# Kernel optimization log

Hardware: AMD Instinct MI355X
Metric: run time of the kernel (lower is better)

## Reference

```python
import jax, jax.numpy as jnp
import numpy as np

LAM = 0.7      # lambda_param
GAM = 2.0      # gamma (weight upper bound)
ALPHA = 0.1    # age modulation scale
FGAM = 0.1     # fusion_gamma
SIGMAS = jnp.array([0.1, 0.5, 1.0, 2.0], dtype=jnp.float32)  # multi-kernel sigmas


def setup_inputs() -> dict:
    key = jax.random.key(0)
    ks = jax.random.split(key, 12)
    B, C, D, H, W, K = 12, 64, 32, 32, 32, 32
    mid, red = C // 2, C // 4
    Z = jax.random.normal(ks[0], (B, C, D, H, W), jnp.float32)
    masks = (jax.random.uniform(ks[1], (K, D, H, W)) > 0.5).astype(jnp.float32)
    masks = masks.at[:, 0, 0, 0].set(1.0)  # guarantee every region non-empty
    labels = jnp.arange(B, dtype=jnp.int32) % 3  # 4 samples each of CN/MCI/AD
    ages = 50.0 + 40.0 * jax.random.uniform(ks[2], (B,), jnp.float32)
    prior_weights = 1.0 + 0.1 * jax.random.normal(ks[3], (K,), jnp.float32)
    struct_w = 0.05 * jax.random.normal(ks[4], (mid, C), jnp.float32)
    noise_w = 0.05 * jax.random.normal(ks[5], (mid, C), jnp.float32)
    up_w = 0.05 * jax.random.normal(ks[6], (C, mid), jnp.float32)
    region_w = 0.05 * jax.random.normal(ks[7], (C, C, 3, 3, 3), jnp.float32)
    m_w1 = 0.05 * jax.random.normal(ks[8], (red, C), jnp.float32)
    m_b1 = jnp.zeros((red,), jnp.float32)
    m_w2 = 0.05 * jax.random.normal(ks[9], (C, red), jnp.float32)
    m_b2 = jnp.zeros((C,), jnp.float32)
    return dict(Z=Z, masks=masks, labels=labels, ages=ages, prior_weights=prior_weights,
                struct_w=struct_w, noise_w=noise_w, up_w=up_w, region_w=region_w,
                m_w1=m_w1, m_b1=m_b1, m_w2=m_w2, m_b2=m_b2)


def _mmd_pair(kern, ca, cb):
    # kern: [S,K,B,B] RBF kernels; ca/cb: [B] float class indicators.
    # Unbiased MMD^2 per region, averaged over sigmas -> [K].
    m = ca.sum()
    n = cb.sum()
    Kaa = jnp.einsum('skij,i,j->sk', kern, ca, ca)
    da = jnp.einsum('skii,i->sk', kern, ca)
    Kbb = jnp.einsum('skij,i,j->sk', kern, cb, cb)
    db = jnp.einsum('skii,i->sk', kern, cb)
    t1 = (Kaa - da) / (m * (m - 1.0))
    t2 = (Kbb - db) / (n * (n - 1.0))
    t3 = jnp.einsum('skij,i,j->sk', kern, ca, cb) * (-2.0 / (m * n))
    return (t1 + t2 + t3).mean(0)


def _forward(Z, masks, labels, ages, prior_weights, struct_w, noise_w, up_w,
             region_w, m_w1, m_b1, m_w2, m_b2):
    B, C = Z.shape[:2]
    K = masks.shape[0]
    # --- region-specific aggregation (fused segment-reduce over masks) ---
    msum = masks.sum((1, 2, 3))                                   # [K]
    rf = jnp.einsum('bcdhw,kdhw->bkc', Z, masks) / (msum[None, :, None] + 1e-6)
    # --- multi-class multi-kernel MMD per region ---
    x2 = jnp.sum(rf * rf, -1)                                     # [B,K]
    ip = jnp.einsum('ikc,jkc->kij', rf, rf)                       # [K,B,B]
    d2 = jnp.maximum(x2.T[:, :, None] + x2.T[:, None, :] - 2.0 * ip, 0.0)
    kern = jnp.exp(-d2[None] / (2.0 * SIGMAS[:, None, None, None] ** 2))  # [S,K,B,B]
    c_cn = (labels == 0).astype(jnp.float32)
    c_mci = (labels == 1).astype(jnp.float32)
    c_ad = (labels == 2).astype(jnp.float32)
    D_mmd = (_mmd_pair(kern, c_ad, c_cn) + _mmd_pair(kern, c_mci, c_cn)
             + _mmd_pair(kern, c_ad, c_mci))                      # [K]
    max_mmd = jnp.maximum(D_mmd.max(), 1e-6)
    nm = jnp.clip(D_mmd / max_mmd, 0.0)
    # symmetric KL between prior and MMD-evidence distributions (batchmean -> /K)
    lp = jax.nn.log_softmax(prior_weights)
    lq = jax.nn.log_softmax(nm)
    p = jnp.exp(lp)
    q = jnp.exp(lq)
    reg = 0.5 * jnp.sum(q * (lq - lp)) / K + 0.5 * jnp.sum(p * (lp - lq)) / K
    # --- prior-guided adaptive spatial weights ---
    base = LAM * prior_weights + (1.0 - LAM) * nm
    af = 1.0 + jax.nn.softplus(ALPHA * (ages - 50.0))             # [B]
    Wk = jax.nn.softmax(jnp.clip(base[None, :] * af[:, None], 0.0, GAM), axis=1)
    spatial = jnp.einsum('bk,kdhw->bdhw', Wk, masks)[:, None]     # [B,1,D,H,W]
    # --- orthogonal decomposition ---
    cs = jnp.einsum('oc,bcdhw->bodhw', struct_w, Z)               # 1x1x1 conv
    cnoise = jnp.einsum('oc,bcdhw->bodhw', noise_w, Z)
    s = cs.reshape(B, cs.shape[1], -1)
    n = cnoise.reshape(B, cnoise.shape[1], -1)
    eps = 1e-8
    cos = jnp.sum(s * n, -1) / (jnp.maximum(jnp.linalg.norm(s, axis=-1), eps)
                                * jnp.maximum(jnp.linalg.norm(n, axis=-1), eps))
    ortho = jnp.abs(cos).mean()
    Z_clean = jnp.einsum('oc,bcdhw->bodhw', up_w, cs)
    # --- region base field + 3x3x3 conv + channel modulation ---
    Zrb = jnp.einsum('bkc,kdhw->bcdhw', rf, masks)
    Zrec = jax.lax.conv_general_dilated(
        Zrb, region_w, (1, 1, 1), 'SAME',
        dimension_numbers=('NCDHW', 'OIDHW', 'NCDHW'))
    h = jax.nn.relu(jnp.einsum('bkc,rc->bkr', rf, m_w1) + m_b1)
    mod = jax.nn.softplus(jnp.einsum('bkr,cr->bkc', h, m_w2) + m_b2)  # [B,K,C]
    Zmod = Zrec * jnp.einsum('bkc,kdhw->bcdhw', mod, masks)
    Z_out = Z_clean + FGAM * (Zmod * spatial)
    return rf, spatial, Z_out, reg + ortho


def reference(Z, masks, labels, ages, prior_weights, struct_w, noise_w, up_w,
              region_w, m_w1, m_b1, m_w2, m_b2):
    return _forward(Z, masks, labels, ages, prior_weights, struct_w, noise_w,
                    up_w, region_w, m_w1, m_b1, m_w2, m_b2)
```

## Files before the change

### kernel.cpp

```cpp
#include <hip/hip_runtime.h>
#include <hip/hip_bf16.h>
#include <math.h>

#define REG_OFF    0
#define ORTHO_OFF  1
#define FLAG_OFF   2
#define MSUM_OFF   4
#define RF_OFF     64
#define G_OFF      24640
#define WKW_OFF    73792
#define MODTB_OFF  74176
#define M1TTH_OFF  86464
#define M1TTL_OFF  88512
#define WKCB_OFF   90560
#define IPK_OFF    422336
#define WS_TOTAL   426944
#define ZERO_FLOATS 73792

#define RF_OUT   0
#define SPAT_OUT 24576
#define ZOUT_OUT 417792
#define SCAL_OUT 25583616

typedef unsigned short u16;
typedef short bh8 __attribute__((ext_vector_type(8)));
typedef float fv4 __attribute__((ext_vector_type(4)));

__device__ __forceinline__ float bf2f(u16 u) {
  union { unsigned int i; float f; } x; x.i = ((unsigned int)u) << 16; return x.f;
}
__device__ __forceinline__ u16 f2bf(float f) {
  unsigned int u = __float_as_uint(f);
  return (u16)((u + 0x7fffu + ((u >> 16) & 1u)) >> 16);
}
__device__ __forceinline__ float ldin(const void* p, size_t i, bool f32) {
  return f32 ? ((const float*)p)[i] : bf2f(((const u16*)p)[i]);
}

__global__ void k_probe(const void* __restrict__ Z, float* __restrict__ ws) {
  int t = threadIdx.x;
  const u16* s = (const u16*)Z;
  float mx = 0.f;
  for (int i = t; i < 8192; i += 256) {
    float a = fabsf(bf2f(s[i]));
    if (!(a < 1e30f)) a = 3e38f;
    mx = fmaxf(mx, a);
  }
  __shared__ float r[256];
  r[t] = mx; __syncthreads();
  for (int o = 128; o > 0; o >>= 1) { if (t < o) r[t] = fmaxf(r[t], r[t + o]); __syncthreads(); }
  if (t == 0) ws[FLAG_OFF] = (r[0] > 1e6f) ? 1.f : 0.f;
}

__global__ void k_msum(const void* __restrict__ masks, float* __restrict__ ws) {
  int k = blockIdx.x, t = threadIdx.x;
  bool f32 = ws[FLAG_OFF] > 0.5f;
  float s = 0.f;
  for (int v = t; v < 32768; v += 256) s += ldin(masks, ((size_t)k << 15) + v, f32);
  __shared__ float red[256];
  red[t] = s; __syncthreads();
  for (int off = 128; off > 0; off >>= 1) { if (t < off) red[t] += red[t + off]; __syncthreads(); }
  if (t == 0) ws[MSUM_OFF + k] = red[0];
}

__global__ __launch_bounds__(256) void k_rfgram(const void* __restrict__ Z,
                                                const void* __restrict__ masks,
                                                float* __restrict__ ws) {
  __shared__ float Zt[64][68];
  __shared__ float Mt[64][36];
  int b = blockIdx.y, t = threadIdx.x;
  bool f32 = ws[FLAG_OFF] > 0.5f;
  int ci = t & 15, gj = t >> 4;
  int c0 = ci << 2, c20 = gj << 2, k0 = gj << 1;
  float accG[16], accR[8];
#pragma unroll
  for (int i = 0; i < 16; i++) accG[i] = 0.f;
#pragma unroll
  for (int i = 0; i < 8; i++) accR[i] = 0.f;
  int vs = blockIdx.x << 9;
  for (int t8 = 0; t8 < 8; t8++) {
    int vb = vs + (t8 << 6);
    __syncthreads();
    if (f32) {
      const float* Zf = (const float*)Z;
      const float* Mf = (const float*)masks;
#pragma unroll
      for (int i = 0; i < 8; i++) {
        int idx = (i << 8) + t, c = idx >> 5, v2 = (idx & 31) << 1;
        float2 u = *(const float2*)(Zf + (((size_t)(b << 6) + c) << 15) + vb + v2);
        Zt[v2][c] = u.x; Zt[v2 + 1][c] = u.y;
      }
#pragma unroll
      for (int i = 0; i < 4; i++) {
        int idx = (i << 8) + t, k = idx >> 5, v2 = (idx & 31) << 1;
        float2 u = *(const float2*)(Mf + ((size_t)k << 15) + vb + v2);
        Mt[v2][k] = u.x; Mt[v2 + 1][k] = u.y;
      }
    } else {
      const u16* Zs = (const u16*)Z;
      const u16* Ms = (const u16*)masks;
#pragma unroll
      for (int i = 0; i < 8; i++) {
        int idx = (i << 8) + t, c = idx >> 5, v2 = (idx & 31) << 1;
        unsigned int u = *(const unsigned int*)(Zs + (((size_t)(b << 6) + c) << 15) + vb + v2);
        Zt[v2][c]     = bf2f((u16)(u & 0xffff));
        Zt[v2 + 1][c] = bf2f((u16)(u >> 16));
      }
#pragma unroll
      for (int i = 0; i < 4; i++) {
        int idx = (i << 8) + t, k = idx >> 5, v2 = (idx & 31) << 1;
        unsigned int u = *(const unsigned int*)(Ms + ((size_t)k << 15) + vb + v2);
        Mt[v2][k]     = bf2f((u16)(u & 0xffff));
        Mt[v2 + 1][k] = bf2f((u16)(u >> 16));
      }
    }
    __syncthreads();
    for (int vt = 0; vt < 64; vt++) {
      float4 z1 = *(const float4*)&Zt[vt][c0];
      float4 z2 = *(const float4*)&Zt[vt][c20];
      float2 m2 = *(const float2*)&Mt[vt][k0];
      float z1a[4] = {z1.x, z1.y, z1.z, z1.w};
      float z2a[4] = {z2.x, z2.y, z2.z, z2.w};
      float m2a[2] = {m2.x, m2.y};
#pragma unroll
      for (int i = 0; i < 4; i++) {
#pragma unroll
        for (int j = 0; j < 4; j++) accG[(i << 2) + j] += z1a[i] * z2a[j];
#pragma unroll
        for (int kk = 0; kk < 2; kk++) accR[(i << 1) + kk] += z1a[i] * m2a[kk];
      }
    }
  }
  float* Gd = ws + G_OFF + (b << 12);
  float* Rd = ws + RF_OFF + (b << 11);
#pragma unroll
  for (int i = 0; i < 4; i++) {
#pragma unroll
    for (int j = 0; j < 4; j++) atomicAdd(Gd + ((c0 + i) << 6) + c20 + j, accG[(i << 2) + j]);
#pragma unroll
    for (int kk = 0; kk < 2; kk++) atomicAdd(Rd + ((k0 + kk) << 6) + c0 + i, accR[(i << 1) + kk]);
  }
}

__global__ void k_scale_rf(float* __restrict__ ws, float* __restrict__ out) {
  int i = blockIdx.x * 256 + threadIdx.x;
  int k = (i >> 6) & 31;
  float v = ws[RF_OFF + i] / (ws[MSUM_OFF + k] + 1e-6f);
  ws[RF_OFF + i] = v;
  out[RF_OUT + i] = v;
}

__global__ void k_ipk(float* __restrict__ ws) {
  __shared__ float rfk[12][65];
  int k = blockIdx.x, t = threadIdx.x;
  for (int i = t; i < 768; i += 256) {
    int b = i >> 6, c = i & 63;
    rfk[b][c] = ws[RF_OFF + (((size_t)(b << 5) + k) << 6) + c];
  }
  __syncthreads();
  if (t < 144) {
    int i = t / 12, j = t - (t / 12) * 12;
    float s = 0.f;
#pragma unroll
    for (int c = 0; c < 64; c++) s += rfk[i][c] * rfk[j][c];
    ws[IPK_OFF + k * 144 + t] = s;
  }
}

__global__ void k_mmdw(const int* __restrict__ labels, const void* __restrict__ ages,
                       const void* __restrict__ prior, float* __restrict__ ws) {
  __shared__ float IPL[32 * 145];
  __shared__ float dpart[128];
  __shared__ float Dm[32], nms[32], bases[32], pwl[32];
  __shared__ int labs[12];
  int t = threadIdx.x;
  bool f32 = ws[FLAG_OFF] > 0.5f;
  if (t < 12) labs[t] = labels[t];
  for (int i = t; i < 4608; i += 256) {
    int k = i / 144, r = i - k * 144;
    IPL[k * 145 + r] = ws[IPK_OFF + i];
  }
  __syncthreads();
  if (t < 128) {
    int k = t >> 2, s = t & 3;
    const float inv2s2[4] = {50.f, 2.f, 0.5f, 0.125f};
    float inv = inv2s2[s];
    const float* pk = IPL + k * 145;
    float c0 = 0.f, c1 = 0.f, c2 = 0.f;
#pragma unroll
    for (int i = 0; i < 12; i++) {
      int li = labs[i];
      c0 += (li == 0) ? 1.f : 0.f;
      c1 += (li == 1) ? 1.f : 0.f;
      c2 += (li == 2) ? 1.f : 0.f;
    }
    float s00=0,s01=0,s02=0,s10=0,s11=0,s12=0,s20=0,s21=0,s22=0;
    float dg0=0, dg1=0, dg2=0;
    for (int i = 0; i < 12; i++) {
      int li = labs[i];
      float x2i = pk[i * 13];
      float r0=0, r1=0, r2=0, dge=0;
      for (int j = 0; j < 12; j++) {
        float d2 = fmaxf(x2i + pk[j * 13] - 2.f * pk[i * 12 + j], 0.f);
        float e = expf(-d2 * inv);
        int lj = labs[j];
        r0 += (lj == 0) ? e : 0.f;
        r1 += (lj == 1) ? e : 0.f;
        r2 += (lj == 2) ? e : 0.f;
        if (j == i) dge = e;
      }
      if (li == 0)      { s00 += r0; s01 += r1; s02 += r2; dg0 += dge; }
      else if (li == 1) { s10 += r0; s11 += r1; s12 += r2; dg1 += dge; }
      else              { s20 += r0; s21 += r1; s22 += r2; dg2 += dge; }
    }
    float ta = (s22 - dg2) / (c2 * (c2 - 1.f));
    float tb = (s00 - dg0) / (c0 * (c0 - 1.f));
    float tc = (s11 - dg1) / (c1 * (c1 - 1.f));
    float dsum = (ta + tb - 2.f * s20 / (c2 * c0))
               + (tc + tb - 2.f * s10 / (c1 * c0))
               + (ta + tc - 2.f * s21 / (c2 * c1));
    dpart[t] = dsum;
  }
  __syncthreads();
  if (t < 32) {
    Dm[t] = (dpart[t * 4] + dpart[t * 4 + 1] + dpart[t * 4 + 2] + dpart[t * 4 + 3]) * 0.25f;
    pwl[t] = (float)ldin(prior, t, f32);
  }
  __syncthreads();
  if (t == 0) {
    float mx = 1e-6f;
    for (int k = 0; k < 32; k++) mx = fmaxf(mx, Dm[k]);
    float nmax = -1e30f, pmax = -1e30f;
    for (int k = 0; k < 32; k++) {
      nms[k] = fmaxf(Dm[k] / mx, 0.f);
      nmax = fmaxf(nmax, nms[k]);
      pmax = fmaxf(pmax, pwl[k]);
    }
    float nse = 0.f, pse = 0.f;
    for (int k = 0; k < 32; k++) { nse += expf(nms[k] - nmax); pse += expf(pwl[k] - pmax); }
    float lns = logf(nse), lps = logf(pse);
    float reg = 0.f;
    for (int k = 0; k < 32; k++) {
      float lqk = nms[k] - nmax - lns;
      float lpk = pwl[k] - pmax - lps;
      reg += 0.5f * (expf(lqk) * (lqk - lpk) + expf(lpk) * (lpk - lqk));
    }
    ws[REG_OFF] = reg / 32.f;
    for (int k = 0; k < 32; k++) bases[k] = 0.7f * pwl[k] + 0.3f * nms[k];
  }
  __syncthreads();
  if (t < 12) {
    float x = 0.1f * (ldin(ages, t, f32) - 50.f);
    float af = 1.f + fmaxf(x, 0.f) + log1pf(expf(-fabsf(x)));
    float w[32];
    float mx = -1e30f;
#pragma unroll
    for (int k = 0; k < 32; k++) {
      float v = fminf(fmaxf(bases[k] * af, 0.f), 2.f);
      w[k] = v; mx = fmaxf(mx, v);
    }
    float se = 0.f;
#pragma unroll
    for (int k = 0; k < 32; k++) se += expf(w[k] - mx);
#pragma unroll
    for (int k = 0; k < 32; k++) ws[WKW_OFF + (t << 5) + k] = expf(w[k] - mx) / se;
  }
}

__global__ __launch_bounds__(64) void k_mod(const void* __restrict__ m_w1, const void* __restrict__ m_b1,
                                            const void* __restrict__ m_w2, const void* __restrict__ m_b2,
                                            float* __restrict__ ws) {
  __shared__ float W1[16][65];
  __shared__ float W2T[16][64];
  __shared__ float B1[16], B2[64], RL[64], H[16];
  int bk = blockIdx.x, t = threadIdx.x;
  int bb = bk >> 5, kk = bk & 31;
  bool f32 = ws[FLAG_OFF] > 0.5f;
  for (int i = t; i < 1024; i += 64) {
    W1[i >> 6][i & 63] = ldin(m_w1, i, f32);
    W2T[i & 15][i >> 4] = ldin(m_w2, i, f32);
  }
  if (t < 16) B1[t] = ldin(m_b1, t, f32);
  B2[t] = ldin(m_b2, t, f32);
  RL[t] = ws[RF_OFF + (bk << 6) + t];
  __syncthreads();
  if (t < 16) {
    float s = B1[t];
#pragma unroll
    for (int c = 0; c < 64; c++) s += RL[c] * W1[t][c];
    H[t] = fmaxf(s, 0.f);
  }
  __syncthreads();
  {
    int c = t;
    float s = B2[c];
#pragma unroll
    for (int rr = 0; rr < 16; rr++) s += H[rr] * W2T[rr][c];
    float mv = fmaxf(s, 0.f) + log1pf(expf(-fabsf(s)));
    ((u16*)(ws + MODTB_OFF))[((size_t)bb * 64 + c) * 32 + kk] = f2bf(mv);
  }
}

__global__ void k_m1t(const void* __restrict__ struct_w, const void* __restrict__ up_w,
                      float* __restrict__ ws) {
  __shared__ float UPT[32][64];
  __shared__ float ST[32][64];
  int t = threadIdx.x, blk = blockIdx.x;
  bool f32 = ws[FLAG_OFF] > 0.5f;
  for (int i = t; i < 2048; i += 256) {
    UPT[i & 31][i >> 5] = ldin(up_w, i, f32);
    ST[i >> 6][i & 63] = ldin(struct_w, i, f32);
  }
  __syncthreads();
  int idx = (blk << 8) + t;
  int cin = idx >> 6, co = idx & 63;
  float s = 0.f;
#pragma unroll
  for (int j = 0; j < 32; j++) s += UPT[j][co] * ST[j][cin];
  u16 hi = f2bf(s);
  ((u16*)(ws + M1TTH_OFF))[co * 64 + cin] = hi;
  ((u16*)(ws + M1TTL_OFF))[co * 64 + cin] = f2bf(s - bf2f(hi));
}

__global__ void k_ortho(const void* __restrict__ sw, const void* __restrict__ nw,
                        float* __restrict__ ws) {
  int b = blockIdx.x >> 5, o = blockIdx.x & 31, c = threadIdx.x;
  bool f32 = ws[FLAG_OFF] > 0.5f;
  const float* Gb = ws + G_OFF + (b << 12);
  float ts = 0.f, tn = 0.f;
  for (int c2 = 0; c2 < 64; c2++) {
    float g = Gb[(c << 6) + c2];
    ts += g * ldin(sw, (o << 6) + c2, f32);
    tn += g * ldin(nw, (o << 6) + c2, f32);
  }
  float swc = ldin(sw, (o << 6) + c, f32);
  float nwc = ldin(nw, (o << 6) + c, f32);
  float ds = swc * tn, ss = swc * ts, nn = nwc * tn;
  for (int off = 32; off > 0; off >>= 1) {
    ds += __shfl_down(ds, off);
    ss += __shfl_down(ss, off);
    nn += __shfl_down(nn, off);
  }
  if (c == 0) {
    ss = fmaxf(ss, 0.f); nn = fmaxf(nn, 0.f);
    float cosv = ds / (fmaxf(sqrtf(ss), 1e-8f) * fmaxf(sqrtf(nn), 1e-8f));
    atomicAdd(ws + ORTHO_OFF, fabsf(cosv) * (1.f / 384.f));
  }
}

__global__ void k_wk(const void* __restrict__ rw, float* __restrict__ ws) {
  int bk = blockIdx.x;
  int b = bk >> 5, k = bk & 31;
  int t = threadIdx.x;
  bool f32 = ws[FLAG_OFF] > 0.5f;
  __shared__ float rl[64];
  if (t < 64) rl[t] = ws[RF_OFF + (bk << 6) + t];
  __syncthreads();
  u16* dst = (u16*)(ws + WKCB_OFF);
  for (int idx = t; idx < 1728; idx += 256) {
    int o = idx / 27, d = idx - o * 27;
    float s = 0.f;
    for (int c = 0; c < 64; c++) s += rl[c] * ldin(rw, (size_t)o * 1728 + c * 27 + d, f32);
    dst[((size_t)b * 64 + o) * 864 + k * 27 + d] = f2bf(s);
  }
}

__global__ void k_spatial(const void* __restrict__ masks, const float* __restrict__ ws,
                          float* __restrict__ out) {
  int b = blockIdx.y, t = threadIdx.x;
  bool f32 = ws[FLAG_OFF] > 0.5f;
  __shared__ float wl[32];
  if (t < 32) wl[t] = ws[WKW_OFF + (b << 5) + t];
  __syncthreads();
  int v0 = (blockIdx.x << 11) + (t << 3);
  float s[8] = {0, 0, 0, 0, 0, 0, 0, 0};
  for (int k = 0; k < 32; k++) {
    float wkv = wl[k];
    float mv[8];
    if (f32) {
      const float* Mf = (const float*)masks + ((size_t)k << 15) + v0;
      float4 a = *(const float4*)Mf, bb = *(const float4*)(Mf + 4);
      mv[0]=a.x; mv[1]=a.y; mv[2]=a.z; mv[3]=a.w; mv[4]=bb.x; mv[5]=bb.y; mv[6]=bb.z; mv[7]=bb.w;
    } else {
      uint4 u = *(const uint4*)((const u16*)masks + ((size_t)k << 15) + v0);
      mv[0]=bf2f((u16)(u.x & 0xffff)); mv[1]=bf2f((u16)(u.x >> 16));
      mv[2]=bf2f((u16)(u.y & 0xffff)); mv[3]=bf2f((u16)(u.y >> 16));
      mv[4]=bf2f((u16)(u.z & 0xffff)); mv[5]=bf2f((u16)(u.z >> 16));
      mv[6]=bf2f((u16)(u.w & 0xffff)); mv[7]=bf2f((u16)(u.w >> 16));
    }
#pragma unroll
    for (int j = 0; j < 8; j++) s[j] += wkv * mv[j];
  }
#pragma unroll
  for (int j = 0; j < 8; j++) out[SPAT_OUT + (b << 15) + v0 + j] = s[j];
}

__global__ __launch_bounds__(256) void k_final(const void* __restrict__ Z,
                                               const void* __restrict__ masks,
                                               const float* __restrict__ ws,
                                               float* __restrict__ out) {
  __shared__ u16 POOL[33024];
  __shared__ float wl[32];
  __shared__ float spl[256];
  u16* MH  = POOL;
  u16* KDK = POOL + 19456;
  u16* KDO = POOL + 20320;
  u16* ZH  = POOL;
  u16* ZL  = POOL + 16512;

  int b = blockIdx.y, tile = blockIdx.x, t = threadIdx.x;
  int lane = t & 63, w = t >> 6;
  int lo16 = lane & 15, g = lane >> 4, g8 = g << 3;
  bool f32 = ws[FLAG_OFF] > 0.5f;
  int d0 = (tile >> 4) << 2, h0 = ((tile >> 2) & 3) << 3, w0 = (tile & 3) << 3;

  for (int i = t; i < 32 * 600; i += 256) {
    int k = i / 600, r = i - k * 600;
    int hd = r / 100, rr = r - hd * 100, hh = rr / 10, hw = rr - hh * 10;
    int gd = d0 - 1 + hd, gh = h0 - 1 + hh, gw = w0 - 1 + hw;
    u16 val = 0;
    if ((unsigned)gd < 32u && (unsigned)gh < 32u && (unsigned)gw < 32u) {
      float mv = ldin(masks, ((size_t)k << 15) + (gd << 10) + (gh << 5) + gw, f32);
      val = (u16)(__float_as_uint(mv) >> 16);
    }
    MH[k * 608 + r] = val;
  }
  for (int i = t; i < 864; i += 256) {
    int k = i / 27, d = i - k * 27;
    int a = d / 9, r9 = d - a * 9, bb = r9 / 3, cc = r9 - bb * 3;
    KDK[i] = (u16)k;
    KDO[i] = (u16)(a * 100 + bb * 10 + cc);
  }
  if (t < 32) wl[t] = ws[WKW_OFF + (b << 5) + t];
  __syncthreads();

  {
    int dz = t >> 6, hy = (t >> 3) & 7, wx = t & 7;
    int hb = dz * 100 + hy * 10 + wx;
    float sp = 0.f;
#pragma unroll
    for (int k = 0; k < 32; k++) sp += wl[k] * bf2f(MH[k * 608 + hb + 111]);
    spl[t] = sp;
  }

  int hb4[4], v4[4];
#pragma unroll
  for (int pt = 0; pt < 4; pt++) {
    int pos = (w << 6) + (pt << 4) + lo16;
    int dz = pos >> 6, hy = (pos >> 3) & 7, wx = pos & 7;
    hb4[pt] = dz * 100 + hy * 10 + wx;
    v4[pt] = ((d0 + dz) << 10) + ((h0 + hy) << 5) + (w0 + wx);
  }

  fv4 acc[4][4];
#pragma unroll
  for (int ot = 0; ot < 4; ot++)
#pragma unroll
    for (int pt = 0; pt < 4; pt++) { acc[ot][pt][0]=0.f; acc[ot][pt][1]=0.f; acc[ot][pt][2]=0.f; acc[ot][pt][3]=0.f; }

  const u16* Wb = (const u16*)(ws + WKCB_OFF) + (size_t)b * 55296;
#pragma unroll 1
  for (int s = 0; s < 27; s++) {
    int kbase = (s << 5) + g8;
    int kk[8], off[8];
#pragma unroll
    for (int j = 0; j < 8; j++) { kk[j] = KDK[kbase + j]; off[j] = KDO[kbase + j]; }
    bh8 a[4];
#pragma unroll
    for (int ot = 0; ot < 4; ot++)
      a[ot] = *(const bh8*)(Wb + ((ot << 4) + lo16) * 864 + kbase);
#pragma unroll
    for (int pt = 0; pt < 4; pt++) {
      bh8 bv;
#pragma unroll
      for (int j = 0; j < 8; j++) bv[j] = (short)MH[kk[j] * 608 + hb4[pt] + off[j]];
#pragma unroll
      for (int ot = 0; ot < 4; ot++)
        acc[ot][pt] = __builtin_amdgcn_mfma_f32_16x16x32_bf16(a[ot], bv, acc[ot][pt], 0, 0, 0);
    }
  }

  {
    const u16* modtb = (const u16*)(ws + MODTB_OFF);
    bh8 am[4];
#pragma unroll
    for (int ot = 0; ot < 4; ot++)
      am[ot] = *(const bh8*)(modtb + ((size_t)b * 64 + (ot << 4) + lo16) * 32 + g8);
    fv4 zero4; zero4[0]=0.f; zero4[1]=0.f; zero4[2]=0.f; zero4[3]=0.f;
#pragma unroll
    for (int pt = 0; pt < 4; pt++) {
      bh8 bc;
#pragma unroll
      for (int j = 0; j < 8; j++) bc[j] = (short)MH[(g8 + j) * 608 + hb4[pt] + 111];
      float spf = 0.1f * spl[(w << 6) + (pt << 4) + lo16];
#pragma unroll
      for (int ot = 0; ot < 4; ot++) {
        fv4 mm = __builtin_amdgcn_mfma_f32_16x16x32_bf16(am[ot], bc, zero4, 0, 0, 0);
        acc[ot][pt] = acc[ot][pt] * mm * spf;
      }
    }
  }
  __syncthreads();

  for (int i = t; i < 16384; i += 256) {
    int c = i >> 8, pos = i & 255;
    int dz = pos >> 6, hy = (pos >> 3) & 7, wx = pos & 7;
    int v = ((d0 + dz) << 10) + ((h0 + hy) << 5) + (w0 + wx);
    float zv = ldin(Z, (((size_t)(b << 6) + c) << 15) + v, f32);
    u16 h = f2bf(zv);
    ZH[c * 258 + pos] = h;
    ZL[c * 258 + pos] = f2bf(zv - bf2f(h));
  }
  __syncthreads();

  {
    const u16* m1tth = (const u16*)(ws + M1TTH_OFF);
    const u16* m1ttl = (const u16*)(ws + M1TTL_OFF);
#pragma unroll 1
    for (int st = 0; st < 2; st++) {
      int cb = (st << 5) + g8;
      bh8 ah[4], al[4];
#pragma unroll
      for (int ot = 0; ot < 4; ot++) {
        ah[ot] = *(const bh8*)(m1tth + ((ot << 4) + lo16) * 64 + cb);
        al[ot] = *(const bh8*)(m1ttl + ((ot << 4) + lo16) * 64 + cb);
      }
#pragma unroll
      for (int pt = 0; pt < 4; pt++) {
        int pcol = (w << 6) + (pt << 4) + lo16;
        bh8 bh, bl;
#pragma unroll
        for (int j = 0; j < 8; j++) {
          bh[j] = (short)ZH[(cb + j) * 258 + pcol];
          bl[j] = (short)ZL[(cb + j) * 258 + pcol];
        }
#pragma unroll
        for (int ot = 0; ot < 4; ot++) {
          acc[ot][pt] = __builtin_amdgcn_mfma_f32_16x16x32_bf16(ah[ot], bh, acc[ot][pt], 0, 0, 0);
          acc[ot][pt] = __builtin_amdgcn_mfma_f32_16x16x32_bf16(ah[ot], bl, acc[ot][pt], 0, 0, 0);
          acc[ot][pt] = __builtin_amdgcn_mfma_f32_16x16x32_bf16(al[ot], bh, acc[ot][pt], 0, 0, 0);
        }
      }
    }
  }

#pragma unroll
  for (int ot = 0; ot < 4; ot++)
#pragma unroll
    for (int pt = 0; pt < 4; pt++)
#pragma unroll
      for (int r = 0; r < 4; r++) {
        int o = (ot << 4) + (g << 2) + r;
        out[(size_t)ZOUT_OUT + (((size_t)(b << 6) + o) << 15) + v4[pt]] = acc[ot][pt][r];
      }
  if ((t | tile | b) == 0) out[SCAL_OUT] = ws[REG_OFF] + ws[ORTHO_OFF];
}

extern "C" void kernel_launch(void* const* d_in, const int* in_sizes, int n_in,
                              void* d_out, int out_size, void* d_ws, size_t ws_size,
                              hipStream_t stream) {
  (void)in_sizes; (void)n_in; (void)out_size; (void)ws_size;
  const void* Z        = d_in[0];
  const void* masks    = d_in[1];
  const int*  labels   = (const int*)d_in[2];
  const void* ages     = d_in[3];
  const void* prior    = d_in[4];
  const void* struct_w = d_in[5];
  const void* noise_w  = d_in[6];
  const void* up_w     = d_in[7];
  const void* region_w = d_in[8];
  const void* m_w1     = d_in[9];
  const void* m_b1     = d_in[10];
  const void* m_w2     = d_in[11];
  const void* m_b2     = d_in[12];
  float* ws = (float*)d_ws;
  float* out = (float*)d_out;

  hipMemsetAsync(d_ws, 0, (size_t)ZERO_FLOATS * 4, stream);
  k_probe<<<1, 256, 0, stream>>>(Z, ws);
  k_msum<<<32, 256, 0, stream>>>(masks, ws);
  k_rfgram<<<dim3(64, 12), 256, 0, stream>>>(Z, masks, ws);
  k_scale_rf<<<96, 256, 0, stream>>>(ws, out);
  k_m1t<<<16, 256, 0, stream>>>(struct_w, up_w, ws);
  k_ipk<<<32, 256, 0, stream>>>(ws);
  k_mmdw<<<1, 256, 0, stream>>>(labels, ages, prior, ws);
  k_mod<<<384, 64, 0, stream>>>(m_w1, m_b1, m_w2, m_b2, ws);
  k_ortho<<<384, 64, 0, stream>>>(struct_w, noise_w, ws);
  k_wk<<<384, 256, 0, stream>>>(region_w, ws);
  k_spatial<<<dim3(16, 12), 256, 0, stream>>>(masks, ws, out);
  k_final<<<dim3(128, 12), 256, 0, stream>>>(Z, masks, ws, out);
}
```

Baseline: 765.8 us.

## Transpose mask halo and conv weights to region-minor layout for vector LDS loads

Stores the haloed mask tile in LDS as position-major with the 32 regions contiguous (stride 40), and reorders the per-sample conv weights so the reduction index is tap-major with region innermost. This replaces eight scalar LDS gathers per MFMA operand, plus the index lookup tables, with a single 16-byte vector load. The Z staging for the 1x1 path is split into two channel halves in a smaller transposed buffer, which shrinks shared memory so the kernel can request three blocks per CU. The trade-off is an extra barrier pair per half and a launch bound that may cap registers.

```diff
diff --git a/kernel.cpp b/kernel.cpp
--- a/kernel.cpp
+++ b/kernel.cpp
@@ -361,7 +361,7 @@
     int o = idx / 27, d = idx - o * 27;
     float s = 0.f;
     for (int c = 0; c < 64; c++) s += rl[c] * ldin(rw, (size_t)o * 1728 + c * 27 + d, f32);
-    dst[((size_t)b * 64 + o) * 864 + k * 27 + d] = f2bf(s);
+    dst[(((size_t)b * 64 + o) * 27 + d) * 32 + k] = f2bf(s);
   }
 }
 
@@ -395,18 +395,17 @@
   for (int j = 0; j < 8; j++) out[SPAT_OUT + (b << 15) + v0 + j] = s[j];
 }
 
-__global__ __launch_bounds__(256) void k_final(const void* __restrict__ Z,
-                                               const void* __restrict__ masks,
-                                               const float* __restrict__ ws,
-                                               float* __restrict__ out) {
-  __shared__ u16 POOL[33024];
+#define MHS 40
+__global__ __launch_bounds__(256, 3) void k_final(const void* __restrict__ Z,
+                                                  const void* __restrict__ masks,
+                                                  const float* __restrict__ ws,
+                                                  float* __restrict__ out) {
+  __shared__ u16 POOL[24000];
   __shared__ float wl[32];
   __shared__ float spl[256];
-  u16* MH  = POOL;
-  u16* KDK = POOL + 19456;
-  u16* KDO = POOL + 20320;
-  u16* ZH  = POOL;
-  u16* ZL  = POOL + 16512;
+  u16* MHT = POOL;
+  u16* ZTH = POOL;
+  u16* ZTL = POOL + 8192;
 
   int b = blockIdx.y, tile = blockIdx.x, t = threadIdx.x;
   int lane = t & 63, w = t >> 6;
@@ -423,23 +422,17 @@
       float mv = ldin(masks, ((size_t)k << 15) + (gd << 10) + (gh << 5) + gw, f32);
       val = (u16)(__float_as_uint(mv) >> 16);
     }
-    MH[k * 608 + r] = val;
-  }
-  for (int i = t; i < 864; i += 256) {
-    int k = i / 27, d = i - k * 27;
-    int a = d / 9, r9 = d - a * 9, bb = r9 / 3, cc = r9 - bb * 3;
-    KDK[i] = (u16)k;
-    KDO[i] = (u16)(a * 100 + bb * 10 + cc);
+    MHT[r * MHS + k] = val;
   }
   if (t < 32) wl[t] = ws[WKW_OFF + (b << 5) + t];
   __syncthreads();
 
   {
     int dz = t >> 6, hy = (t >> 3) & 7, wx = t & 7;
-    int hb = dz * 100 + hy * 10 + wx;
+    const u16* cen = MHT + (dz * 100 + hy * 10 + wx + 111) * MHS;
     float sp = 0.f;
 #pragma unroll
-    for (int k = 0; k < 32; k++) sp += wl[k] * bf2f(MH[k * 608 + hb + 111]);
+    for (int k = 0; k < 32; k++) sp += wl[k] * bf2f(cen[k]);
     spl[t] = sp;
   }
 
@@ -459,21 +452,17 @@
     for (int pt = 0; pt < 4; pt++) { acc[ot][pt][0]=0.f; acc[ot][pt][1]=0.f; acc[ot][pt][2]=0.f; acc[ot][pt][3]=0.f; }
 
   const u16* Wb = (const u16*)(ws + WKCB_OFF) + (size_t)b * 55296;
-#pragma unroll 1
-  for (int s = 0; s < 27; s++) {
-    int kbase = (s << 5) + g8;
-    int kk[8], off[8];
-#pragma unroll
-    for (int j = 0; j < 8; j++) { kk[j] = KDK[kbase + j]; off[j] = KDO[kbase + j]; }
+#pragma unroll 3
+  for (int d = 0; d < 27; d++) {
+    int da = d / 9, r9 = d - da * 9, db = r9 / 3, dc = r9 - db * 3;
+    int off = da * 100 + db * 10 + dc;
     bh8 a[4];
 #pragma unroll
     for (int ot = 0; ot < 4; ot++)
-      a[ot] = *(const bh8*)(Wb + ((ot << 4) + lo16) * 864 + kbase);
+      a[ot] = *(const bh8*)(Wb + ((ot << 4) + lo16) * 864 + (d << 5) + g8);
 #pragma unroll
     for (int pt = 0; pt < 4; pt++) {
-      bh8 bv;
-#pragma unroll
-      for (int j = 0; j < 8; j++) bv[j] = (short)MH[kk[j] * 608 + hb4[pt] + off[j]];
+      bh8 bv = *(const bh8*)(MHT + (hb4[pt] + off) * MHS + g8);
 #pragma unroll
       for (int ot = 0; ot < 4; ot++)
         acc[ot][pt] = __builtin_amdgcn_mfma_f32_16x16x32_bf16(a[ot], bv, acc[ot][pt], 0, 0, 0);
@@ -489,9 +478,7 @@
     fv4 zero4; zero4[0]=0.f; zero4[1]=0.f; zero4[2]=0.f; zero4[3]=0.f;
 #pragma unroll
     for (int pt = 0; pt < 4; pt++) {
-      bh8 bc;
-#pragma unroll
-      for (int j = 0; j < 8; j++) bc[j] = (short)MH[(g8 + j) * 608 + hb4[pt] + 111];
+      bh8 bc = *(const bh8*)(MHT + (hb4[pt] + 111) * MHS + g8);
       float spf = 0.1f * spl[(w << 6) + (pt << 4) + lo16];
 #pragma unroll
       for (int ot = 0; ot < 4; ot++) {
@@ -500,46 +487,46 @@
       }
     }
   }
-  __syncthreads();
-
-  for (int i = t; i < 16384; i += 256) {
-    int c = i >> 8, pos = i & 255;
-    int dz = pos >> 6, hy = (pos >> 3) & 7, wx = pos & 7;
-    int v = ((d0 + dz) << 10) + ((h0 + hy) << 5) + (w0 + wx);
-    float zv = ldin(Z, (((size_t)(b << 6) + c) << 15) + v, f32);
-    u16 h = f2bf(zv);
-    ZH[c * 258 + pos] = h;
-    ZL[c * 258 + pos] = f2bf(zv - bf2f(h));
-  }
-  __syncthreads();
-
-  {
-    const u16* m1tth = (const u16*)(ws + M1TTH_OFF);
-    const u16* m1ttl = (const u16*)(ws + M1TTL_OFF);
+
+  const u16* m1tth = (const u16*)(ws + M1TTH_OFF);
+  const u16* m1ttl = (const u16*)(ws + M1TTL_OFF);
+  int dzs = t >> 6, hys = (t >> 3) & 7, wxs = t & 7;
+  int vstage = ((d0 + dzs) << 10) + ((h0 + hys) << 5) + (w0 + wxs);
 #pragma unroll 1
-    for (int st = 0; st < 2; st++) {
-      int cb = (st << 5) + g8;
-      bh8 ah[4], al[4];
+  for (int st = 0; st < 2; st++) {
+    int cb = st << 5;
+    __syncthreads();
+#pragma unroll
+    for (int gg = 0; gg < 4; gg++) {
+      bh8 hb, lb;
+#pragma unroll
+      for (int j = 0; j < 8; j++) {
+        int c = cb + (gg << 3) + j;
+        float zv = ldin(Z, (((size_t)(b << 6) + c) << 15) + vstage, f32);
+        u16 h = f2bf(zv);
+        hb[j] = (short)h;
+        lb[j] = (short)f2bf(zv - bf2f(h));
+      }
+      *(bh8*)(ZTH + (((gg << 8) + t) << 3)) = hb;
+      *(bh8*)(ZTL + (((gg << 8) + t) << 3)) = lb;
+    }
+    __syncthreads();
+    bh8 ah[4], al[4];
+#pragma unroll
+    for (int ot = 0; ot < 4; ot++) {
+      ah[ot] = *(const bh8*)(m1tth + ((ot << 4) + lo16) * 64 + cb + g8);
+      al[ot] = *(const bh8*)(m1ttl + ((ot << 4) + lo16) * 64 + cb + g8);
+    }
+#pragma unroll
+    for (int pt = 0; pt < 4; pt++) {
+      int pcol = (w << 6) + (pt << 4) + lo16;
+      bh8 bh = *(const bh8*)(ZTH + (((g << 8) + pcol) << 3));
+      bh8 bl = *(const bh8*)(ZTL + (((g << 8) + pcol) << 3));
 #pragma unroll
       for (int ot = 0; ot < 4; ot++) {
-        ah[ot] = *(const bh8*)(m1tth + ((ot << 4) + lo16) * 64 + cb);
-        al[ot] = *(const bh8*)(m1ttl + ((ot << 4) + lo16) * 64 + cb);
-      }
-#pragma unroll
-      for (int pt = 0; pt < 4; pt++) {
-        int pcol = (w << 6) + (pt << 4) + lo16;
-        bh8 bh, bl;
-#pragma unroll
-        for (int j = 0; j < 8; j++) {
-          bh[j] = (short)ZH[(cb + j) * 258 + pcol];
-          bl[j] = (short)ZL[(cb + j) * 258 + pcol];
-        }
-#pragma unroll
-        for (int ot = 0; ot < 4; ot++) {
-          acc[ot][pt] = __builtin_amdgcn_mfma_f32_16x16x32_bf16(ah[ot], bh, acc[ot][pt], 0, 0, 0);
-          acc[ot][pt] = __builtin_amdgcn_mfma_f32_16x16x32_bf16(ah[ot], bl, acc[ot][pt], 0, 0, 0);
-          acc[ot][pt] = __builtin_amdgcn_mfma_f32_16x16x32_bf16(al[ot], bh, acc[ot][pt], 0, 0, 0);
-        }
+        acc[ot][pt] = __builtin_amdgcn_mfma_f32_16x16x32_bf16(ah[ot], bh, acc[ot][pt], 0, 0, 0);
+        acc[ot][pt] = __builtin_amdgcn_mfma_f32_16x16x32_bf16(ah[ot], bl, acc[ot][pt], 0, 0, 0);
+        acc[ot][pt] = __builtin_amdgcn_mfma_f32_16x16x32_bf16(al[ot], bh, acc[ot][pt], 0, 0, 0);
       }
     }
   }
```

Result: faster. 693.5 us (-9.4%).
